# Kernel tuning notes

Measured on AMD Instinct MI355X. Metric: run time of the kernel, lower is better.

## Reference

```python
import jax, jax.numpy as jnp
import numpy as np

N_QUBITS = 4
N_FEATURES = 16
B = 1048576


def _bcast(theta):
    # theta: scalar or [B]; make broadcastable against [B,2,2,2] amp slices
    return theta if jnp.ndim(theta) == 0 else theta.reshape(theta.shape[0], 1, 1, 1)


def apply_ry(state, theta, w):
    # state: [B,2,2,2,2] complex; RY(theta) on wire w
    th = _bcast(theta)
    c = jnp.cos(th / 2).astype(state.dtype)
    s = jnp.sin(th / 2).astype(state.dtype)
    st = jnp.moveaxis(state, w + 1, -1)
    a0, a1 = st[..., 0], st[..., 1]
    st = jnp.stack([c * a0 - s * a1, s * a0 + c * a1], axis=-1)
    return jnp.moveaxis(st, -1, w + 1)


def apply_rz(state, theta, w):
    # RZ(theta) = diag(e^{-i theta/2}, e^{+i theta/2}) on wire w
    th = _bcast(theta)
    ph = jnp.exp(-0.5j * th.astype(jnp.float32)).astype(state.dtype)
    st = jnp.moveaxis(state, w + 1, -1)
    a0, a1 = st[..., 0], st[..., 1]
    st = jnp.stack([ph * a0, jnp.conj(ph) * a1], axis=-1)
    return jnp.moveaxis(st, -1, w + 1)


def cnot(state, c, t):
    st = jnp.moveaxis(state, (c + 1, t + 1), (-2, -1))  # [...,2(ctrl),2(tgt)]
    st = jnp.stack([st[..., 0, :], st[..., 1, ::-1]], axis=-2)
    return jnp.moveaxis(st, (-2, -1), (c + 1, t + 1))


def quantum_encoder_batched(x, qw):
    # x: [B,16] float32, qw: [8] float32 -> latents [B,4] (PauliZ expvals)
    b = x.shape[0]
    state = jnp.zeros((b, 16), jnp.complex64).at[:, 0].set(1.0)
    state = state.reshape(b, 2, 2, 2, 2)
    pi = jnp.float32(np.pi)
    for i in range(N_QUBITS):
        state = apply_ry(state, x[:, i] * pi, i)
        state = apply_rz(state, x[:, i + N_QUBITS] * pi, i)
    for i in range(N_QUBITS - 1):
        state = cnot(state, i, i + 1)
    for i in range(N_QUBITS):
        state = apply_ry(state, qw[2 * i], i)
        state = apply_rz(state, qw[2 * i + 1], i)
    for i in range(N_QUBITS - 1):
        state = cnot(state, i, i + 1)
    probs = state.real ** 2 + state.imag ** 2  # [B,2,2,2,2]
    zs = []
    for i in range(N_QUBITS):
        axes = tuple(a for a in range(1, N_QUBITS + 1) if a != i + 1)
        p = probs.sum(axes)  # [B,2]
        zs.append(p[:, 0] - p[:, 1])
    return jnp.stack(zs, axis=1)  # [B,4]


def setup_inputs() -> dict:
    key = jax.random.key(0)
    ks = jax.random.split(key, 8)
    x = jax.random.uniform(ks[0], (B, N_FEATURES), dtype=jnp.float32)
    q_weights = 0.01 * jax.random.normal(ks[1], (2 * N_QUBITS,), dtype=jnp.float32)
    # decoder: Linear(4,16) -> ReLU -> Linear(16,32) -> ReLU -> Linear(32,16)
    W1 = jax.random.normal(ks[2], (16, 4), dtype=jnp.float32) / jnp.sqrt(4.0)
    b1 = jnp.zeros((16,), jnp.float32)
    W2 = jax.random.normal(ks[3], (32, 16), dtype=jnp.float32) / jnp.sqrt(16.0)
    b2 = jnp.zeros((32,), jnp.float32)
    W3 = jax.random.normal(ks[4], (16, 32), dtype=jnp.float32) / jnp.sqrt(32.0)
    b3 = jnp.zeros((16,), jnp.float32)
    return {"x": x, "q_weights": q_weights, "W1": W1, "b1": b1,
            "W2": W2, "b2": b2, "W3": W3, "b3": b3}


def reference(x, q_weights, W1, b1, W2, b2, W3, b3):
    z = quantum_encoder_batched(x, q_weights)          # [B,4]
    h = jax.nn.relu(z @ W1.T + b1)                      # [B,16]
    h = jax.nn.relu(h @ W2.T + b2)                      # [B,32]
    return h @ W3.T + b3                                # [B,16]
```

## Files before the change

kernel.cpp:

```cpp
#include <hip/hip_runtime.h>

using u16 = unsigned short;
using u32 = unsigned int;
typedef float v2f   __attribute__((ext_vector_type(2)));
typedef float f32x4 __attribute__((ext_vector_type(4)));
typedef short s16x8 __attribute__((ext_vector_type(8)));

union FragU { u32 d[4]; s16x8 s; uint4 q; };

__device__ __forceinline__ u32 cvt_pk_bf16(float a, float b) {
    u32 r;
    asm("v_cvt_pk_bf16_f32 %0, %1, %2" : "=v"(r) : "v"(a), "v"(b));
    return r;
}
__device__ __forceinline__ void split2(float w0, float w1, u32& hi, u32& lo) {
    u32 u0 = __float_as_uint(w0), u1 = __float_as_uint(w1);
    hi = (u0 >> 16) | (u1 & 0xFFFF0000u);
    float r0 = w0 - __uint_as_float(u0 & 0xFFFF0000u);
    float r1 = w1 - __uint_as_float(u1 & 0xFFFF0000u);
    lo = cvt_pk_bf16(r0, r1);
}
__device__ __forceinline__ u32 bp(int ib, u32 v) {
    return (u32)__builtin_amdgcn_ds_bpermute(ib, (int)v);
}
__device__ __forceinline__ v2f pkfma(v2f a, v2f b, v2f c) { return __builtin_elementwise_fma(a, b, c); }
__device__ __forceinline__ v2f s2v(float x) { return (v2f){x, x}; }
__device__ __forceinline__ f32x4 tov(float4 v) { return (f32x4){v.x, v.y, v.z, v.w}; }
#define MFMA16 __builtin_amdgcn_mfma_f32_16x16x32_bf16

__global__ void __launch_bounds__(256) qae_bperm(
    const float* __restrict__ x,  const float* __restrict__ qw,
    const float* __restrict__ W1, const float* __restrict__ b1,
    const float* __restrict__ W2, const float* __restrict__ b2,
    const float* __restrict__ W3, const float* __restrict__ b3,
    float* __restrict__ out, int n)
{
    int tid  = threadIdx.x;
    int b    = blockIdx.x * 256 + tid;
    int bc   = b < n ? b : n - 1;
    int lane = tid & 63;
    int wid  = tid >> 6;
    int vn   = lane & 15, vq = lane >> 4;
    int gbase = blockIdx.x * 256 + (tid - lane);

    __shared__ uint4 shfrag[5][64];

    const float4* xf = reinterpret_cast<const float4*>(x);
    float4 xa = xf[(size_t)bc * 4];
    float4 xc = xf[(size_t)bc * 4 + 1];

    bool q0 = (vq == 0), q1v = (vq == 1), qlt2 = (vq < 2);

    if (wid == 0) {
        float4 w = reinterpret_cast<const float4*>(W1)[vn];
        u32 h0, l0, h1, l1; split2(w.x, w.y, h0, l0); split2(w.z, w.w, h1, l1);
        u32 d0 = q0 ? h0 : (q1v ? l0 : 0);
        u32 d1 = q0 ? h1 : (q1v ? l1 : 0);
        shfrag[0][lane] = make_uint4(d0, d1, 0, 0);
    } else if (wid == 1) {
        const float4* p0 = reinterpret_cast<const float4*>(W2 + vn * 16 + (vq & 1) * 8);
        float4 a0 = p0[0], a1 = p0[1];
        u32 h, l; uint4 H;
        split2(a0.x, a0.y, h, l); H.x = qlt2 ? h : l;
        split2(a0.z, a0.w, h, l); H.y = qlt2 ? h : l;
        split2(a1.x, a1.y, h, l); H.z = qlt2 ? h : l;
        split2(a1.z, a1.w, h, l); H.w = qlt2 ? h : l;
        shfrag[1][lane] = H;
    } else if (wid == 2) {
        const float4* p1 = reinterpret_cast<const float4*>(W2 + (16 + vn) * 16 + (vq & 1) * 8);
        float4 c0 = p1[0], c1v = p1[1];
        u32 h, l; uint4 H;
        split2(c0.x, c0.y, h, l);   H.x = qlt2 ? h : l;
        split2(c0.z, c0.w, h, l);   H.y = qlt2 ? h : l;
        split2(c1v.x, c1v.y, h, l); H.z = qlt2 ? h : l;
        split2(c1v.z, c1v.w, h, l); H.w = qlt2 ? h : l;
        shfrag[2][lane] = H;
    } else {
        const float4* p3 = reinterpret_cast<const float4*>(W3 + vn * 32 + vq * 8);
        float4 e0 = p3[0], e1 = p3[1];
        u32 h, l; uint4 H, L;
        split2(e0.x, e0.y, h, l); H.x = h; L.x = l;
        split2(e0.z, e0.w, h, l); H.y = h; L.y = l;
        split2(e1.x, e1.y, h, l); H.z = h; L.z = l;
        split2(e1.z, e1.w, h, l); H.w = h; L.w = l;
        shfrag[3][lane] = H; shfrag[4][lane] = L;
    }

    float th[4]  = { xa.x, xa.y, xa.z, xa.w };
    float phv[4] = { xc.x, xc.y, xc.z, xc.w };
    float c4[4], u1r[4], u1i[4];
    #pragma unroll
    for (int i = 0; i < 4; ++i) {
        float c  = __builtin_amdgcn_cosf(th[i]  * 0.25f);
        float s  = __builtin_amdgcn_sinf(th[i]  * 0.25f);
        float cz = __builtin_amdgcn_cosf(phv[i] * 0.5f);
        float sz = __builtin_amdgcn_sinf(phv[i] * 0.5f);
        c4[i] = c; u1r[i] = s * cz; u1i[i] = s * sz;
    }
    float p01r[4], p01i[4], p23r[4], p23i[4];
    p01r[0] = c4[0] * c4[1];                          p01i[0] = 0.f;
    p01r[1] = c4[0] * u1r[1];                         p01i[1] = c4[0] * u1i[1];
    p01r[2] = u1r[0] * c4[1];                         p01i[2] = u1i[0] * c4[1];
    p01r[3] = u1r[0] * u1r[1] - u1i[0] * u1i[1];
    p01i[3] = u1r[0] * u1i[1] + u1i[0] * u1r[1];
    p23r[0] = c4[2] * c4[3];                          p23i[0] = 0.f;
    p23r[1] = c4[2] * u1r[3];                         p23i[1] = c4[2] * u1i[3];
    p23r[2] = u1r[2] * c4[3];                         p23i[2] = u1i[2] * c4[3];
    p23r[3] = u1r[2] * u1r[3] - u1i[2] * u1i[3];
    p23i[3] = u1r[2] * u1i[3] + u1i[2] * u1r[3];

    v2f amp[16];
    #pragma unroll
    for (int i = 0; i < 16; ++i) {
        int q0i=(i>>3)&1, q1i=(i>>2)&1, q2i=(i>>1)&1, q3i=i&1;
        int g = (q0i<<3) | ((q1i^q0i)<<2) | ((q2i^q1i)<<1) | (q3i^q2i);
        int hi = g >> 2, lo = g & 3;
        float r, im;
        if (hi == 0) {
            if (lo == 0) { r = p01r[0] * p23r[0];  im = 0.f; }
            else         { r = p01r[0] * p23r[lo]; im = p01r[0] * p23i[lo]; }
        } else if (lo == 0) {
            r = p01r[hi] * p23r[0]; im = p01i[hi] * p23r[0];
        } else {
            r  = p01r[hi] * p23r[lo] - p01i[hi] * p23i[lo];
            im = p01r[hi] * p23i[lo] + p01i[hi] * p23r[lo];
        }
        amp[i] = (v2f){ r, im };
    }
    const float INV4PI = 0.07957747154594767f;
    #pragma unroll
    for (int w = 0; w < 4; ++w) {
        float a = qw[2 * w];
        v2f vc = s2v(__builtin_amdgcn_cosf(a * INV4PI));
        v2f vs = s2v(__builtin_amdgcn_sinf(a * INV4PI));
        int stride = 1 << (3 - w);
        #pragma unroll
        for (int m = 0; m < 16; ++m) {
            if (m & stride) continue;
            int i0 = m, i1 = m | stride;
            v2f a0 = amp[i0], a1 = amp[i1];
            amp[i0] = pkfma(vc, a0, -(vs * a1));
            amp[i1] = pkfma(vc, a1,  (vs * a0));
        }
    }
    v2f Pv[16];
    #pragma unroll
    for (int i = 0; i < 16; ++i) {
        int q0i=(i>>3)&1, q1i=(i>>2)&1, q2i=(i>>1)&1, q3i=i&1;
        int g = (q0i<<3) | ((q1i^q0i)<<2) | ((q2i^q1i)<<1) | (q3i^q2i);
        Pv[i] = amp[g] * amp[g];
    }
    v2f q2[8], q4[4];
    #pragma unroll
    for (int j = 0; j < 8; ++j) q2[j] = Pv[2*j] + Pv[2*j+1];
    #pragma unroll
    for (int j = 0; j < 4; ++j) q4[j] = q2[2*j] + q2[2*j+1];
    v2f z0v = (q4[0] + q4[1]) - (q4[2] + q4[3]);
    v2f z1v = (q4[0] - q4[1]) + (q4[2] - q4[3]);
    v2f z2v = (q2[0]-q2[1]) + (q2[2]-q2[3]) + (q2[4]-q2[5]) + (q2[6]-q2[7]);
    v2f z3v = (Pv[0]-Pv[1]) + (Pv[2]-Pv[3]) + (Pv[4]-Pv[5]) + (Pv[6]-Pv[7])
            + (Pv[8]-Pv[9]) + (Pv[10]-Pv[11]) + (Pv[12]-Pv[13]) + (Pv[14]-Pv[15]);
    float zv0 = z0v.x + z0v.y, zv1 = z1v.x + z1v.y;
    float zv2 = z2v.x + z2v.y, zv3 = z3v.x + z3v.y;

    u32 zd0 = cvt_pk_bf16(zv0, zv1);
    u32 zd1 = cvt_pk_bf16(zv2, zv3);

    __syncthreads();
    FragU A1, A2a, A2b, A3h, A3l;
    A1.q  = shfrag[0][lane];
    A2a.q = shfrag[1][lane];
    A2b.q = shfrag[2][lane];
    A3h.q = shfrag[3][lane];
    A3l.q = shfrag[4][lane];

    float4 c1b  = reinterpret_cast<const float4*>(b1)[vq];
    float4 c2b0 = reinterpret_cast<const float4*>(b2)[vq];
    float4 c2b1 = reinterpret_cast<const float4*>(b2)[4 + vq];
    float4 c3b  = reinterpret_cast<const float4*>(b3)[vq];

    int i2a = ((((2 * vq)    ) & 3) * 16 + vn) * 4;
    int i2b = ((((2 * vq) + 1) & 3) * 16 + vn) * 4;

    #pragma unroll
    for (int t = 0; t < 4; ++t) {
        int viL = (t * 16 + vn) * 4;
        FragU B1; B1.d[0] = bp(viL, zd0); B1.d[1] = bp(viL, zd1); B1.d[2] = 0; B1.d[3] = 0;
        f32x4 c1 = tov(c1b);
        c1 = MFMA16(A1.s, B1.s, c1, 0, 0, 0);
        u32 da0 = cvt_pk_bf16(fmaxf(c1[0], 0.f), fmaxf(c1[1], 0.f));
        u32 da1 = cvt_pk_bf16(fmaxf(c1[2], 0.f), fmaxf(c1[3], 0.f));

        FragU B2;
        B2.d[0] = bp(i2a, da0); B2.d[1] = bp(i2a, da1);
        B2.d[2] = bp(i2b, da0); B2.d[3] = bp(i2b, da1);
        f32x4 ca = tov(c2b0), cb = tov(c2b1);
        ca = MFMA16(A2a.s, B2.s, ca, 0, 0, 0);
        cb = MFMA16(A2b.s, B2.s, cb, 0, 0, 0);
        u32 ea0 = cvt_pk_bf16(fmaxf(ca[0],0.f), fmaxf(ca[1],0.f));
        u32 ea1 = cvt_pk_bf16(fmaxf(ca[2],0.f), fmaxf(ca[3],0.f));
        u32 eb0 = cvt_pk_bf16(fmaxf(cb[0],0.f), fmaxf(cb[1],0.f));
        u32 eb1 = cvt_pk_bf16(fmaxf(cb[2],0.f), fmaxf(cb[3],0.f));

        u32 s0a = bp(i2a, ea0), s0b = bp(i2a, eb0);
        u32 s1a = bp(i2a, ea1), s1b = bp(i2a, eb1);
        u32 s2_ = bp(i2b, ea0), s2b = bp(i2b, eb0);
        u32 s3a = bp(i2b, ea1), s3b = bp(i2b, eb1);
        FragU B3;
        B3.d[0] = qlt2 ? s0a : s0b;
        B3.d[1] = qlt2 ? s1a : s1b;
        B3.d[2] = qlt2 ? s2_ : s2b;
        B3.d[3] = qlt2 ? s3a : s3b;
        f32x4 c3 = tov(c3b);
        c3 = MFMA16(A3l.s, B3.s, c3, 0, 0, 0);
        c3 = MFMA16(A3h.s, B3.s, c3, 0, 0, 0);

        int R = gbase + t * 16 + vn;
        if (R < n)
            *reinterpret_cast<float4*>(out + (size_t)R * 16 + vq * 4) =
                make_float4(c3[0], c3[1], c3[2], c3[3]);
    }
}

extern "C" void kernel_launch(void* const* d_in, const int* in_sizes, int n_in,
                              void* d_out, int out_size, void* d_ws, size_t ws_size,
                              hipStream_t stream) {
    const float* x  = (const float*)d_in[0];
    const float* qw = (const float*)d_in[1];
    const float* W1 = (const float*)d_in[2];
    const float* b1 = (const float*)d_in[3];
    const float* W2 = (const float*)d_in[4];
    const float* b2 = (const float*)d_in[5];
    const float* W3 = (const float*)d_in[6];
    const float* b3 = (const float*)d_in[7];
    float* out = (float*)d_out;

    int n = in_sizes[0] / 16;
    int blocks = (n + 255) / 256;
    qae_bperm<<<blocks, 256, 0, stream>>>(x, qw, W1, b1, W2, b2, W3, b3, out, n);
}
```

Before: 128.1 us.

## Compute PauliZ expectations in closed form via Bloch-vector algebra instead of statevector

Replaces the explicit 16-amplitude complex statevector simulation (build, four RY rotations, CNOT permutation, probability reduction) with closed-form expressions for the four PauliZ expectation values. These are written as products of per-qubit Bloch components and the cosines and sines of the weight angles. This removes most of the per-thread FLOPs and register pressure in the encoder stage. The cost is a hand-derived formula whose correctness depends on the algebra being exact, and rounding will differ slightly from the reference.

```diff
diff --git a/kernel.cpp b/kernel.cpp
--- a/kernel.cpp
+++ b/kernel.cpp
@@ -2,7 +2,6 @@
 
 using u16 = unsigned short;
 using u32 = unsigned int;
-typedef float v2f   __attribute__((ext_vector_type(2)));
 typedef float f32x4 __attribute__((ext_vector_type(4)));
 typedef short s16x8 __attribute__((ext_vector_type(8)));
 
@@ -23,8 +22,6 @@
 __device__ __forceinline__ u32 bp(int ib, u32 v) {
     return (u32)__builtin_amdgcn_ds_bpermute(ib, (int)v);
 }
-__device__ __forceinline__ v2f pkfma(v2f a, v2f b, v2f c) { return __builtin_elementwise_fma(a, b, c); }
-__device__ __forceinline__ v2f s2v(float x) { return (v2f){x, x}; }
 __device__ __forceinline__ f32x4 tov(float4 v) { return (f32x4){v.x, v.y, v.z, v.w}; }
 #define MFMA16 __builtin_amdgcn_mfma_f32_16x16x32_bf16
 
@@ -88,80 +85,44 @@
 
     float th[4]  = { xa.x, xa.y, xa.z, xa.w };
     float phv[4] = { xc.x, xc.y, xc.z, xc.w };
-    float c4[4], u1r[4], u1i[4];
+    float Zb[4], Xb[4], Yb[4];
     #pragma unroll
     for (int i = 0; i < 4; ++i) {
-        float c  = __builtin_amdgcn_cosf(th[i]  * 0.25f);
-        float s  = __builtin_amdgcn_sinf(th[i]  * 0.25f);
-        float cz = __builtin_amdgcn_cosf(phv[i] * 0.5f);
-        float sz = __builtin_amdgcn_sinf(phv[i] * 0.5f);
-        c4[i] = c; u1r[i] = s * cz; u1i[i] = s * sz;
-    }
-    float p01r[4], p01i[4], p23r[4], p23i[4];
-    p01r[0] = c4[0] * c4[1];                          p01i[0] = 0.f;
-    p01r[1] = c4[0] * u1r[1];                         p01i[1] = c4[0] * u1i[1];
-    p01r[2] = u1r[0] * c4[1];                         p01i[2] = u1i[0] * c4[1];
-    p01r[3] = u1r[0] * u1r[1] - u1i[0] * u1i[1];
-    p01i[3] = u1r[0] * u1i[1] + u1i[0] * u1r[1];
-    p23r[0] = c4[2] * c4[3];                          p23i[0] = 0.f;
-    p23r[1] = c4[2] * u1r[3];                         p23i[1] = c4[2] * u1i[3];
-    p23r[2] = u1r[2] * c4[3];                         p23i[2] = u1i[2] * c4[3];
-    p23r[3] = u1r[2] * u1r[3] - u1i[2] * u1i[3];
-    p23i[3] = u1r[2] * u1i[3] + u1i[2] * u1r[3];
-
-    v2f amp[16];
+        float ct = __builtin_amdgcn_cosf(th[i]  * 0.5f);
+        float st = __builtin_amdgcn_sinf(th[i]  * 0.5f);
+        float cp = __builtin_amdgcn_cosf(phv[i] * 0.5f);
+        float sp = __builtin_amdgcn_sinf(phv[i] * 0.5f);
+        Zb[i] = ct; Xb[i] = st * cp; Yb[i] = st * sp;
+    }
+    const float INV2PI = 0.15915494309189535f;
+    float CA[4], SA[4];
     #pragma unroll
-    for (int i = 0; i < 16; ++i) {
-        int q0i=(i>>3)&1, q1i=(i>>2)&1, q2i=(i>>1)&1, q3i=i&1;
-        int g = (q0i<<3) | ((q1i^q0i)<<2) | ((q2i^q1i)<<1) | (q3i^q2i);
-        int hi = g >> 2, lo = g & 3;
-        float r, im;
-        if (hi == 0) {
-            if (lo == 0) { r = p01r[0] * p23r[0];  im = 0.f; }
-            else         { r = p01r[0] * p23r[lo]; im = p01r[0] * p23i[lo]; }
-        } else if (lo == 0) {
-            r = p01r[hi] * p23r[0]; im = p01i[hi] * p23r[0];
-        } else {
-            r  = p01r[hi] * p23r[lo] - p01i[hi] * p23i[lo];
-            im = p01r[hi] * p23i[lo] + p01i[hi] * p23r[lo];
-        }
-        amp[i] = (v2f){ r, im };
-    }
-    const float INV4PI = 0.07957747154594767f;
-    #pragma unroll
-    for (int w = 0; w < 4; ++w) {
-        float a = qw[2 * w];
-        v2f vc = s2v(__builtin_amdgcn_cosf(a * INV4PI));
-        v2f vs = s2v(__builtin_amdgcn_sinf(a * INV4PI));
-        int stride = 1 << (3 - w);
-        #pragma unroll
-        for (int m = 0; m < 16; ++m) {
-            if (m & stride) continue;
-            int i0 = m, i1 = m | stride;
-            v2f a0 = amp[i0], a1 = amp[i1];
-            amp[i0] = pkfma(vc, a0, -(vs * a1));
-            amp[i1] = pkfma(vc, a1,  (vs * a0));
-        }
-    }
-    v2f Pv[16];
-    #pragma unroll
-    for (int i = 0; i < 16; ++i) {
-        int q0i=(i>>3)&1, q1i=(i>>2)&1, q2i=(i>>1)&1, q3i=i&1;
-        int g = (q0i<<3) | ((q1i^q0i)<<2) | ((q2i^q1i)<<1) | (q3i^q2i);
-        Pv[i] = amp[g] * amp[g];
-    }
-    v2f q2[8], q4[4];
-    #pragma unroll
-    for (int j = 0; j < 8; ++j) q2[j] = Pv[2*j] + Pv[2*j+1];
-    #pragma unroll
-    for (int j = 0; j < 4; ++j) q4[j] = q2[2*j] + q2[2*j+1];
-    v2f z0v = (q4[0] + q4[1]) - (q4[2] + q4[3]);
-    v2f z1v = (q4[0] - q4[1]) + (q4[2] - q4[3]);
-    v2f z2v = (q2[0]-q2[1]) + (q2[2]-q2[3]) + (q2[4]-q2[5]) + (q2[6]-q2[7]);
-    v2f z3v = (Pv[0]-Pv[1]) + (Pv[2]-Pv[3]) + (Pv[4]-Pv[5]) + (Pv[6]-Pv[7])
-            + (Pv[8]-Pv[9]) + (Pv[10]-Pv[11]) + (Pv[12]-Pv[13]) + (Pv[14]-Pv[15]);
-    float zv0 = z0v.x + z0v.y, zv1 = z1v.x + z1v.y;
-    float zv2 = z2v.x + z2v.y, zv3 = z3v.x + z3v.y;
+    for (int v = 0; v < 4; ++v) {
+        float a = qw[2 * v] * INV2PI;
+        CA[v] = __builtin_amdgcn_cosf(a);
+        SA[v] = __builtin_amdgcn_sinf(a);
+    }
+    float K00 = CA[0]*CA[1], K10 = SA[0]*CA[1], K01 = CA[0]*SA[1], K11 = SA[0]*SA[1];
+    float L00 = CA[2]*CA[3], L10 = SA[2]*CA[3], L01 = CA[2]*SA[3], L11 = SA[2]*SA[3];
+    float X01 = Xb[0]*Xb[1], Y01 = Yb[0]*Yb[1];
+    float X23 = Xb[2]*Xb[3], Y23 = Yb[2]*Yb[3];
+
+    float zv0 = CA[0]*Zb[0] - SA[0]*X01;
+    float zv1 = K00*Zb[1] - K01*(Zb[0]*Xb[1]*Xb[2]) + K10*Y01 + K11*(Xb[0]*Xb[2]);
+    float t2a =  CA[2]*(Zb[0]*Zb[2])        - SA[2]*(Zb[1]*X23);
+    float t2b = -CA[2]*(X01*Zb[2])          - SA[2]*(Y01*X23);
+    float t2c =  CA[2]*(Yb[1]*Yb[2])        + SA[2]*(Zb[0]*Xb[1]*Xb[3]);
+    float t2d = -CA[2]*(Yb[0]*Zb[1]*Yb[2])  - SA[2]*(Xb[0]*Xb[3]);
+    float zv2 = K00*t2a + K10*t2b + K01*t2c + K11*t2d;
+    float t3a =  L00*(Zb[1]*Zb[3])              + L10*(Zb[0]*Y23)
+               - L01*(Zb[0]*Zb[2]*Xb[3])        + L11*(Zb[1]*Xb[2]);
+    float t3b =  L00*(Y01*Zb[3])                - L10*(X01*Y23)
+               + L01*(X01*Zb[2]*Xb[3])          + L11*(Y01*Xb[2]);
+    float t3c = -L00*(Zb[0]*Xb[1]*Xb[2]*Zb[3])  - L10*(Yb[1]*Zb[2]*Yb[3])
+               - L01*(Yb[1]*Yb[2]*Xb[3])        - L11*(Zb[0]*Xb[1]);
+    float t3d =  L00*(Xb[0]*Xb[2]*Zb[3])        + L10*(Yb[0]*Zb[1]*Zb[2]*Yb[3])
+               + L01*(Yb[0]*Zb[1]*Yb[2]*Xb[3])  + L11*Xb[0];
+    float zv3 = K00*t3a + K10*t3b + K01*t3c + K11*t3d;
 
     u32 zd0 = cvt_pk_bf16(zv0, zv1);
     u32 zd1 = cvt_pk_bf16(zv2, zv3);
```

Measured after the change: 125.4 us. 2.1% less time.
